# Kernel tuning notes

Hardware: AMD Instinct MI355X
Metric: run time of the kernel (lower is better)

## Reference

```python
import jax, jax.numpy as jnp
import numpy as np

B, S, H = 1, 4096, 3584
NQ, NKV, D = 16, 8, 256
N_REP = NQ // NKV  # GQA repeat factor = 2
WINDOW = 2048
SOFTCAP = 50.0
THETA = 10000.0
SCALE = D ** -0.5


def rotate_half(x):
    h = x.shape[-1] // 2
    return jnp.concatenate([-x[..., h:], x[..., :h]], axis=-1)


def setup_inputs() -> dict:
    key = jax.random.key(0)
    k0, k1, k2, k3, k4 = jax.random.split(key, 5)
    return {
        "hidden_states": jax.random.normal(k0, (B, S, H), jnp.float32),
        "wq": jax.random.normal(k1, (H, NQ * D), jnp.float32) / np.sqrt(H).astype(np.float32),
        "wk": jax.random.normal(k2, (H, NKV * D), jnp.float32) / np.sqrt(H).astype(np.float32),
        "wv": jax.random.normal(k3, (H, NKV * D), jnp.float32) / np.sqrt(H).astype(np.float32),
        "wo": jax.random.normal(k4, (NQ * D, H), jnp.float32) / np.sqrt(NQ * D).astype(np.float32),
        "position_ids": jnp.arange(S, dtype=jnp.int64 if jax.config.jax_enable_x64 else jnp.int32)[None, :],
    }


def reference(hidden_states, wq, wk, wv, wo, position_ids):
    b, s, h = hidden_states.shape
    # QKV projections (no bias, per attention_bias=False)
    q = (hidden_states @ wq).reshape(b, s, NQ, D).transpose(0, 2, 1, 3)   # [b, nq, s, d]
    k = (hidden_states @ wk).reshape(b, s, NKV, D).transpose(0, 2, 1, 3)  # [b, nkv, s, d]
    v = (hidden_states @ wv).reshape(b, s, NKV, D).transpose(0, 2, 1, 3)

    # Rotary embeddings (Gemma2RotaryEmbedding): freqs duplicated, rotate_half form
    pos = position_ids.astype(jnp.float32)                         # [b, s]
    inv_freq = 1.0 / (THETA ** (jnp.arange(0, D, 2, dtype=jnp.float32) / D))  # [d/2]
    freqs = pos[..., None] * inv_freq                              # [b, s, d/2]
    emb = jnp.concatenate([freqs, freqs], axis=-1)                 # [b, s, d]
    cos = jnp.cos(emb)[:, None, :, :]                              # [b, 1, s, d]
    sin = jnp.sin(emb)[:, None, :, :]
    q = q * cos + rotate_half(q) * sin
    k = k * cos + rotate_half(k) * sin

    # GQA: repeat_kv (repeat_interleave over head dim)
    k = jnp.repeat(k, N_REP, axis=1)  # [b, nq, s, d]
    v = jnp.repeat(v, N_REP, axis=1)

    # scaled scores + logit softcapping
    scores = jnp.einsum('bhqd,bhkd->bhqk', q, k) * SCALE
    scores = SOFTCAP * jnp.tanh(scores / SOFTCAP)

    # causal + sliding-window mask built from positions
    qpos = position_ids[:, None, :, None]  # [b,1,s,1]
    kpos = position_ids[:, None, None, :]  # [b,1,1,s]
    visible = (kpos <= qpos) & (kpos > qpos - WINDOW)
    scores = jnp.where(visible, scores, jnp.finfo(scores.dtype).min)

    attn = jax.nn.softmax(scores, axis=-1)
    out = jnp.einsum('bhqk,bhkd->bhqd', attn, v)      # [b, nq, s, d]
    out = out.transpose(0, 2, 1, 3).reshape(b, s, NQ * D)
    return out @ wo                                    # [b, s, h]
```

## Files before the change

kernel.cpp:

```cpp
#include <hip/hip_runtime.h>
#include <hip/hip_bf16.h>
#include <cstdint>
#include <cstddef>

#define DEVFN __device__ __forceinline__

typedef __attribute__((ext_vector_type(4))) float f32x4;
typedef __attribute__((ext_vector_type(8))) short bf16x8;
typedef __attribute__((ext_vector_type(4))) short short4v;

static constexpr int S = 4096;
static constexpr int H = 3584;
static constexpr int NQ = 16;
static constexpr int NKV = 8;
static constexpr int D = 256;
static constexpr int WINDOW = 2048;
static constexpr float SCALE = 0.0625f;

DEVFN unsigned short f2bf(float f) {
  union { float f; uint32_t u; } x; x.f = f;
  uint32_t u = x.u;
  u += 0x7fffu + ((u >> 16) & 1u);
  return (unsigned short)(u >> 16);
}
DEVFN float bf2f(unsigned short h) {
  union { uint32_t u; float f; } x; x.u = ((uint32_t)h) << 16;
  return x.f;
}

DEVFN void load_lds16(const void* g, void* l) {
  __builtin_amdgcn_global_load_lds((const __attribute__((address_space(1))) void*)g,
                                   (__attribute__((address_space(3))) void*)l,
                                   16, 0, 0);
}

__global__ __launch_bounds__(256) void cast_hs_kernel(const float* __restrict__ in,
                                                      unsigned short* __restrict__ out) {
  int i = (blockIdx.x * 256 + threadIdx.x) * 4;
  float4 v = *(const float4*)(in + i);
  short4v o;
  o[0] = (short)f2bf(v.x); o[1] = (short)f2bf(v.y);
  o[2] = (short)f2bf(v.z); o[3] = (short)f2bf(v.w);
  *(short4v*)(out + i) = o;
}

__global__ void transpose_cast_kernel(const float* __restrict__ in, unsigned short* __restrict__ out,
                                      int rows, int cols, int out_ld) {
  __shared__ float tile[32][33];
  int r0 = blockIdx.y * 32, c0 = blockIdx.x * 32;
  int tx = threadIdx.x, ty = threadIdx.y;
#pragma unroll
  for (int j = 0; j < 32; j += 8)
    tile[ty + j][tx] = in[(size_t)(r0 + ty + j) * cols + (c0 + tx)];
  __syncthreads();
#pragma unroll
  for (int j = 0; j < 32; j += 8)
    out[(size_t)(c0 + ty + j) * out_ld + (r0 + tx)] = f2bf(tile[tx][ty + j]);
}

__global__ __launch_bounds__(256) void rope_table_kernel(float* __restrict__ cs) {
  int idx = blockIdx.x * 256 + threadIdx.x;
  int s = idx >> 7, i = idx & 127;
  float inv = 1.0f / powf(10000.0f, (float)i * (1.0f / 128.0f));
  float f = (float)s * inv;
  cs[idx] = cosf(f);
  cs[(S * 128) + idx] = sinf(f);
}

__global__ __launch_bounds__(256) void rope_apply_kernel(unsigned short* __restrict__ q,
                                                         unsigned short* __restrict__ k,
                                                         const float* __restrict__ cs) {
  int idx = blockIdx.x * 256 + threadIdx.x;
  int i4 = (idx & 31) * 4;
  int s = (idx >> 5) & (S - 1);
  int hh = idx >> 17;
  unsigned short* base = (hh < NQ) ? (q + ((size_t)hh * S + s) * D)
                                   : (k + ((size_t)(hh - NQ) * S + s) * D);
  float4 c  = *(const float4*)(cs + (s << 7) + i4);
  float4 sn = *(const float4*)(cs + (S * 128) + (s << 7) + i4);
  short4v a = *(short4v*)(base + i4);
  short4v b = *(short4v*)(base + i4 + 128);
  short4v o1, o2;
  o1[0] = (short)f2bf(bf2f((unsigned short)a[0]) * c.x - bf2f((unsigned short)b[0]) * sn.x);
  o1[1] = (short)f2bf(bf2f((unsigned short)a[1]) * c.y - bf2f((unsigned short)b[1]) * sn.y);
  o1[2] = (short)f2bf(bf2f((unsigned short)a[2]) * c.z - bf2f((unsigned short)b[2]) * sn.z);
  o1[3] = (short)f2bf(bf2f((unsigned short)a[3]) * c.w - bf2f((unsigned short)b[3]) * sn.w);
  o2[0] = (short)f2bf(bf2f((unsigned short)b[0]) * c.x + bf2f((unsigned short)a[0]) * sn.x);
  o2[1] = (short)f2bf(bf2f((unsigned short)b[1]) * c.y + bf2f((unsigned short)a[1]) * sn.y);
  o2[2] = (short)f2bf(bf2f((unsigned short)b[2]) * c.z + bf2f((unsigned short)a[2]) * sn.z);
  o2[3] = (short)f2bf(bf2f((unsigned short)b[3]) * c.w + bf2f((unsigned short)a[3]) * sn.w);
  *(short4v*)(base + i4) = o1;
  *(short4v*)(base + i4 + 128) = o2;
}

DEVFN void gemm256_mainloop(const unsigned short* __restrict__ A,
                            const unsigned short* __restrict__ Bt,
                            int Kdim, int lda, int ldb, int row0, int col0,
                            char* lds, f32x4 acc[8][4]) {
  const int tid = threadIdx.x, lane = tid & 63;
  const int w = tid >> 6;
  const int wm = w >> 2, wn = w & 3;
  const int NT = Kdim >> 6;

  const int u = ((tid & 7) * 16) ^ (((tid >> 3) & 7) << 4);
  const int srow = (tid >> 3) + (u >> 6) * 128;
  const int sc = (u & 63) >> 1;

  const unsigned short* aSrc = A + (size_t)(row0 + srow) * lda + sc;
  const unsigned short* bSrc = Bt + (size_t)(col0 + srow) * ldb + sc;
  const size_t aj = (size_t)64 * lda, bj = (size_t)64 * ldb;

  char* const dA = lds + tid * 16;
  char* const dB = lds + 32768 + tid * 16;

  const int aoff = (lane & 15) * 128 + ((((lane >> 4) * 16) + wm * 64) ^ ((lane & 7) << 4));
  const int boff = ((wn & 1) * 64 + (lane & 15)) * 128 +
                   ((((lane >> 4) * 16) + (wn >> 1) * 64) ^ ((lane & 7) << 4));

#define STAGE_A(kt2, kh) do { \
    char* d_ = dA + (((kt2) & 1) << 16) + ((kh) << 14); \
    const unsigned short* s_ = aSrc + (kt2) * 64 + (kh) * 32; \
    load_lds16(s_, d_); load_lds16(s_ + aj, d_ + 8192); } while (0)
#define STAGE_B(kt2, kh) do { \
    char* d_ = dB + (((kt2) & 1) << 16) + ((kh) << 14); \
    const unsigned short* s_ = bSrc + (kt2) * 64 + (kh) * 32; \
    load_lds16(s_, d_); load_lds16(s_ + bj, d_ + 8192); } while (0)

  STAGE_A(0, 0); STAGE_B(0, 0); STAGE_A(0, 1); STAGE_B(0, 1);
  if (NT > 1) { STAGE_A(1, 0); STAGE_B(1, 0); }
  asm volatile("s_waitcnt vmcnt(4)" ::: "memory");
  __builtin_amdgcn_s_barrier();
  asm volatile("" ::: "memory");

  for (int kt = 0; kt < NT; ++kt) {
    const char* lA = lds + ((kt & 1) << 16) + aoff;
    const char* lB = lds + ((kt & 1) << 16) + 32768 + boff;
    bf16x8 bfr[4];
#pragma unroll
    for (int ph = 0; ph < 4; ++ph) {
      const int kh = ph >> 1;
      const int mh = ph & 1;
      bf16x8 af[4];
#pragma unroll
      for (int j = 0; j < 4; ++j)
        af[j] = *(const bf16x8*)(lA + (kh << 14) + (mh * 4 + j) * 2048);
      if (mh == 0) {
#pragma unroll
        for (int n = 0; n < 4; ++n)
          bfr[n] = *(const bf16x8*)(lB + (kh << 14) + n * 2048);
      }
      if (ph == 0)      { if (kt + 1 < NT) STAGE_A(kt + 1, 1); }
      else if (ph == 1) { if (kt + 1 < NT) STAGE_B(kt + 1, 1); }
      else if (ph == 2) { if (kt + 2 < NT) STAGE_A(kt + 2, 0); }
      else              { if (kt + 2 < NT) STAGE_B(kt + 2, 0); }

      asm volatile("" ::: "memory");
      __builtin_amdgcn_s_barrier();
      asm volatile("" ::: "memory");
      __builtin_amdgcn_s_setprio(1);
#pragma unroll
      for (int j = 0; j < 4; ++j)
#pragma unroll
        for (int n = 0; n < 4; ++n)
          acc[mh * 4 + j][n] =
              __builtin_amdgcn_mfma_f32_16x16x32_bf16(af[j], bfr[n], acc[mh * 4 + j][n], 0, 0, 0);
      __builtin_amdgcn_s_setprio(0);
      if (ph == 3) {
        if (kt < NT - 2) asm volatile("s_waitcnt vmcnt(4)" ::: "memory");
        else             asm volatile("s_waitcnt vmcnt(0)" ::: "memory");
      }
      asm volatile("" ::: "memory");
      __builtin_amdgcn_s_barrier();
      asm volatile("" ::: "memory");
    }
  }
#undef STAGE_A
#undef STAGE_B
}

__global__ __launch_bounds__(512, 2) void gemm_qkv_kernel(const unsigned short* __restrict__ A,
                                                          const unsigned short* __restrict__ Bt,
                                                          unsigned short* __restrict__ qb,
                                                          unsigned short* __restrict__ kbuf,
                                                          unsigned short* __restrict__ vtb) {
  extern __shared__ char lds[];
  int bid = blockIdx.x;
  bid = (bid & 7) * 64 + (bid >> 3);
  const int bx = bid & 15, by = bid >> 4;
  const int row0 = bx * 256, col0 = by * 256;
  f32x4 acc[8][4];
  f32x4 z = {0.f, 0.f, 0.f, 0.f};
#pragma unroll
  for (int m = 0; m < 8; ++m)
#pragma unroll
    for (int n = 0; n < 4; ++n) acc[m][n] = z;

  gemm256_mainloop(A, Bt, H, H, H, row0, col0, lds, acc);

  const int lane = threadIdx.x & 63, w = threadIdx.x >> 6;
  const int wm = w >> 2, wn = w & 3;
  const int rbase = row0 + wm * 128 + (lane >> 4) * 4;
  const int cbase = col0 + wn * 64 + (lane & 15);
  if (col0 < 4096) {
#pragma unroll
    for (int m = 0; m < 8; ++m)
#pragma unroll
      for (int n = 0; n < 4; ++n)
#pragma unroll
        for (int r = 0; r < 4; ++r) {
          int row = rbase + m * 16 + r;
          int col = cbase + n * 16;
          qb[((size_t)(col >> 8) * S + row) * D + (col & 255)] = f2bf(acc[m][n][r]);
        }
  } else if (col0 < 6144) {
#pragma unroll
    for (int m = 0; m < 8; ++m)
#pragma unroll
      for (int n = 0; n < 4; ++n)
#pragma unroll
        for (int r = 0; r < 4; ++r) {
          int row = rbase + m * 16 + r;
          int c2 = cbase + n * 16 - 4096;
          kbuf[((size_t)(c2 >> 8) * S + row) * D + (c2 & 255)] = f2bf(acc[m][n][r]);
        }
  } else {
#pragma unroll
    for (int m = 0; m < 8; ++m)
#pragma unroll
      for (int n = 0; n < 4; ++n)
#pragma unroll
        for (int r = 0; r < 4; ++r) {
          int row = rbase + m * 16 + r;
          int c3 = cbase + n * 16 - 6144;
          vtb[((size_t)(c3 >> 8) * D + (c3 & 255)) * S + row] = f2bf(acc[m][n][r]);
        }
  }
}

__global__ __launch_bounds__(512, 2) void gemm_out_kernel(const unsigned short* __restrict__ A,
                                                          const unsigned short* __restrict__ Bt,
                                                          float* __restrict__ C) {
  extern __shared__ char lds[];
  int bid = blockIdx.x;
  bid = (bid & 7) * 28 + (bid >> 3);
  const int bx = bid & 15, by = bid >> 4;
  const int row0 = bx * 256, col0 = by * 256;
  f32x4 acc[8][4];
  f32x4 z = {0.f, 0.f, 0.f, 0.f};
#pragma unroll
  for (int m = 0; m < 8; ++m)
#pragma unroll
    for (int n = 0; n < 4; ++n) acc[m][n] = z;

  gemm256_mainloop(A, Bt, NQ * D, NQ * D, NQ * D, row0, col0, lds, acc);

  const int lane = threadIdx.x & 63, w = threadIdx.x >> 6;
  const int wm = w >> 2, wn = w & 3;
  const int rbase = row0 + wm * 128 + (lane >> 4) * 4;
  const int cbase = col0 + wn * 64 + (lane & 15);
#pragma unroll
  for (int m = 0; m < 8; ++m)
#pragma unroll
    for (int n = 0; n < 4; ++n)
#pragma unroll
      for (int r = 0; r < 4; ++r)
        C[(size_t)(rbase + m * 16 + r) * H + cbase + n * 16] = acc[m][n][r];
}

__global__ __launch_bounds__(256) void attn_kernel(const unsigned short* __restrict__ q,
                                                   const unsigned short* __restrict__ kk_,
                                                   const unsigned short* __restrict__ vt,
                                                   unsigned short* __restrict__ aout) {
  __shared__ __align__(16) char kl[2][16384];
  __shared__ __align__(16) char vl[2][16384];
  __shared__ __align__(16) char pl[4096];
  const int tid = threadIdx.x, lane = tid & 63, w = tid >> 6;
  const int h = blockIdx.y, hv = h >> 1;
  const int q0 = blockIdx.x * 64;
  const int ql = lane & 15;
  const int grp = lane >> 4;
  const int qg = q0 + w * 16 + ql;

  bf16x8 qf[8];
  const unsigned short* qrow = q + ((size_t)h * S + qg) * D;
#pragma unroll
  for (int t = 0; t < 8; ++t)
    qf[t] = *(const bf16x8*)(qrow + t * 32 + grp * 8);

  f32x4 oacc[16];
  f32x4 z = {0.f, 0.f, 0.f, 0.f};
#pragma unroll
  for (int i = 0; i < 16; ++i) oacc[i] = z;
  float lrun = 0.0f;

  int lo = q0 - (WINDOW - 1); if (lo < 0) lo = 0;
  const int kb0 = lo & ~31;
  const int kend = q0 + 32;

  const unsigned short* kbase = kk_ + (size_t)hv * S * D;
  const unsigned short* vbase = vt + (size_t)hv * D * S;
  int koff[4], voff[4];
#pragma unroll
  for (int j = 0; j < 4; ++j) {
    int c = w + 4 * j;
    int key = c * 2 + (lane >> 5);
    int colK = (((lane & 31) * 16) ^ ((key & 7) << 4)) >> 1;
    koff[j] = key * D + colK;
    int dd = c * 16 + (lane >> 2);
    int colV = (((lane & 3) * 16) ^ (((dd >> 1) & 3) << 4)) >> 1;
    voff[j] = dd * S + colV;
  }

  auto stage = [&](int buf, int kb) {
#pragma unroll
    for (int j = 0; j < 4; ++j) {
      int c = w + 4 * j;
      load_lds16(kbase + (size_t)kb * D + koff[j], &kl[buf][c * 1024]);
      load_lds16(vbase + kb + voff[j], &vl[buf][c * 1024]);
    }
  };

  stage(0, kb0);
  int cur = 0;
  const int psw = ((ql >> 1) & 3) << 4;
  char* pw = pl + w * 1024;

  for (int kb = kb0; kb <= kend; kb += 32) {
    __syncthreads();
    if (kb + 32 <= kend) stage(cur ^ 1, kb + 32);

    f32x4 sacc[2];
    sacc[0] = z; sacc[1] = z;
#pragma unroll
    for (int mt = 0; mt < 2; ++mt) {
      const int krow = mt * 16 + ql;
      const char* kbp = kl[cur] + krow * 512;
      const int sw = (krow & 7) << 4;
#pragma unroll
      for (int t = 0; t < 8; ++t) {
        bf16x8 a = *(const bf16x8*)(kbp + ((t * 64 + grp * 16) ^ sw));
        sacc[mt] = __builtin_amdgcn_mfma_f32_16x16x32_bf16(a, qf[t], sacc[mt], 0, 0, 0);
      }
    }

    float pv[8];
#pragma unroll
    for (int i = 0; i < 8; ++i) {
      float x = sacc[i >> 2][i & 3];
      float e = __expf(x * (SCALE / 25.0f));
      float rc = __builtin_amdgcn_rcpf(e + 1.0f);
      pv[i] = __expf(rc * -100.0f);
    }
    if (kb + 31 > q0) {
#pragma unroll
      for (int i = 0; i < 8; ++i) {
        int key = kb + (i >> 2) * 16 + grp * 4 + (i & 3);
        if (key > qg) pv[i] = 0.0f;
      }
    } else if (kb < q0 - (WINDOW - 64)) {
#pragma unroll
      for (int i = 0; i < 8; ++i) {
        int key = kb + (i >> 2) * 16 + grp * 4 + (i & 3);
        if (key <= qg - WINDOW) pv[i] = 0.0f;
      }
    }
#pragma unroll
    for (int i = 0; i < 8; ++i) lrun += pv[i];

#pragma unroll
    for (int mt = 0; mt < 2; ++mt) {
      short4v pk;
      pk[0] = (short)f2bf(pv[mt * 4 + 0]);
      pk[1] = (short)f2bf(pv[mt * 4 + 1]);
      pk[2] = (short)f2bf(pv[mt * 4 + 2]);
      pk[3] = (short)f2bf(pv[mt * 4 + 3]);
      *(short4v*)(pw + ql * 64 + ((mt * 32 + grp * 8) ^ psw)) = pk;
    }
    asm volatile("s_waitcnt lgkmcnt(0)" ::: "memory");
    bf16x8 pb = *(const bf16x8*)(pw + ql * 64 + ((grp * 16) ^ psw));

#pragma unroll
    for (int nt = 0; nt < 16; ++nt) {
      int dr = nt * 16 + ql;
      bf16x8 va = *(const bf16x8*)(vl[cur] + dr * 64 + ((grp * 16) ^ (((dr >> 1) & 3) << 4)));
      oacc[nt] = __builtin_amdgcn_mfma_f32_16x16x32_bf16(va, pb, oacc[nt], 0, 0, 0);
    }
    cur ^= 1;
  }

  lrun += __shfl_xor(lrun, 16);
  lrun += __shfl_xor(lrun, 32);
  lrun = fmaxf(lrun, 1e-35f);
  float rl = 1.0f / lrun;
  unsigned short* orow = aout + (size_t)qg * (NQ * D) + h * D;
#pragma unroll
  for (int nt = 0; nt < 16; ++nt) {
    short4v o;
    o[0] = (short)f2bf(oacc[nt][0] * rl);
    o[1] = (short)f2bf(oacc[nt][1] * rl);
    o[2] = (short)f2bf(oacc[nt][2] * rl);
    o[3] = (short)f2bf(oacc[nt][3] * rl);
    *(short4v*)(orow + nt * 16 + grp * 4) = o;
  }
}

extern "C" void kernel_launch(void* const* d_in, const int* in_sizes, int n_in,
                              void* d_out, int out_size, void* d_ws, size_t ws_size,
                              hipStream_t stream) {
  const float* hs = (const float*)d_in[0];
  const float* wq = (const float*)d_in[1];
  const float* wk = (const float*)d_in[2];
  const float* wv = (const float*)d_in[3];
  const float* wo = (const float*)d_in[4];
  float* out = (float*)d_out;

  char* ws = (char*)d_ws;
  size_t off = 0;
  auto alloc = [&](size_t bytes) {
    char* p = ws + off;
    off += (bytes + 255) & ~(size_t)255;
    return p;
  };
  unsigned short* hsb   = (unsigned short*)alloc((size_t)S * H * 2);
  unsigned short* wqkvT = (unsigned short*)alloc((size_t)8192 * H * 2);
  unsigned short* woT   = (unsigned short*)alloc((size_t)H * 4096 * 2);
  unsigned short* qb    = (unsigned short*)alloc((size_t)NQ * S * D * 2);
  unsigned short* kbuf  = (unsigned short*)alloc((size_t)NKV * S * D * 2);
  unsigned short* vtb   = (unsigned short*)alloc((size_t)NKV * D * S * 2);
  unsigned short* aob   = (unsigned short*)alloc((size_t)S * NQ * D * 2);
  float*          cs    = (float*)alloc((size_t)S * 128 * 2 * 4);
  if (off > ws_size) return;

  dim3 tb(32, 8);
  cast_hs_kernel<<<(S * H) / 1024, 256, 0, stream>>>(hs, hsb);
  transpose_cast_kernel<<<dim3(4096 / 32, H / 32), tb, 0, stream>>>(wq, wqkvT, H, 4096, H);
  transpose_cast_kernel<<<dim3(2048 / 32, H / 32), tb, 0, stream>>>(wk, wqkvT + (size_t)4096 * H, H, 2048, H);
  transpose_cast_kernel<<<dim3(2048 / 32, H / 32), tb, 0, stream>>>(wv, wqkvT + (size_t)6144 * H, H, 2048, H);
  transpose_cast_kernel<<<dim3(H / 32, 4096 / 32), tb, 0, stream>>>(wo, woT, 4096, H, 4096);
  rope_table_kernel<<<(S * 128) / 256, 256, 0, stream>>>(cs);
  gemm_qkv_kernel<<<512, 512, 131072, stream>>>(hsb, wqkvT, qb, kbuf, vtb);
  rope_apply_kernel<<<((NQ + NKV) * S * 32) / 256, 256, 0, stream>>>(qb, kbuf, cs);
  attn_kernel<<<dim3(S / 64, NQ), 256, 0, stream>>>(qb, kbuf, vtb, aob);
  gemm_out_kernel<<<224, 512, 131072, stream>>>(aob, woT, out);
}
```

Measured before the change: 650.3 us.

## Double query rows per attention block to reuse K/V tiles across two query subtiles

Each attention block now covers 128 queries instead of 64, and each wave processes two 16-row query subtiles. Every K and V fragment read from LDS feeds MFMAs for both subtiles, which halves K/V global traffic and LDS reads per query. The costs are higher register pressure from two output accumulator sets (launch_bounds now requests 2 blocks per SIMD), half as many blocks in the grid, and more wasted work on fully masked tiles because the key range per block is wider.

```diff
diff --git a/kernel.cpp b/kernel.cpp
--- a/kernel.cpp
+++ b/kernel.cpp
@@ -267,35 +267,40 @@
         C[(size_t)(rbase + m * 16 + r) * H + cbase + n * 16] = acc[m][n][r];
 }
 
-__global__ __launch_bounds__(256) void attn_kernel(const unsigned short* __restrict__ q,
-                                                   const unsigned short* __restrict__ kk_,
-                                                   const unsigned short* __restrict__ vt,
-                                                   unsigned short* __restrict__ aout) {
+__global__ __launch_bounds__(256, 2) void attn_kernel(const unsigned short* __restrict__ q,
+                                                      const unsigned short* __restrict__ kk_,
+                                                      const unsigned short* __restrict__ vt,
+                                                      unsigned short* __restrict__ aout) {
   __shared__ __align__(16) char kl[2][16384];
   __shared__ __align__(16) char vl[2][16384];
-  __shared__ __align__(16) char pl[4096];
+  __shared__ __align__(16) char pl[8192];
   const int tid = threadIdx.x, lane = tid & 63, w = tid >> 6;
   const int h = blockIdx.y, hv = h >> 1;
-  const int q0 = blockIdx.x * 64;
+  const int q0 = blockIdx.x * 128;
   const int ql = lane & 15;
   const int grp = lane >> 4;
-  const int qg = q0 + w * 16 + ql;
-
-  bf16x8 qf[8];
-  const unsigned short* qrow = q + ((size_t)h * S + qg) * D;
-#pragma unroll
-  for (int t = 0; t < 8; ++t)
-    qf[t] = *(const bf16x8*)(qrow + t * 32 + grp * 8);
-
-  f32x4 oacc[16];
+  const int qw = q0 + w * 32;
+
+  bf16x8 qf[2][8];
+#pragma unroll
+  for (int qs = 0; qs < 2; ++qs) {
+    const unsigned short* qrow = q + ((size_t)h * S + qw + qs * 16 + ql) * D;
+#pragma unroll
+    for (int t = 0; t < 8; ++t)
+      qf[qs][t] = *(const bf16x8*)(qrow + t * 32 + grp * 8);
+  }
+
+  f32x4 oacc[2][16];
   f32x4 z = {0.f, 0.f, 0.f, 0.f};
 #pragma unroll
-  for (int i = 0; i < 16; ++i) oacc[i] = z;
-  float lrun = 0.0f;
+  for (int qs = 0; qs < 2; ++qs)
+#pragma unroll
+    for (int i = 0; i < 16; ++i) oacc[qs][i] = z;
+  float lrun[2] = {0.0f, 0.0f};
 
   int lo = q0 - (WINDOW - 1); if (lo < 0) lo = 0;
   const int kb0 = lo & ~31;
-  const int kend = q0 + 32;
+  const int kend = q0 + 96;
 
   const unsigned short* kbase = kk_ + (size_t)hv * S * D;
   const unsigned short* vbase = vt + (size_t)hv * D * S;
@@ -323,84 +328,99 @@
   stage(0, kb0);
   int cur = 0;
   const int psw = ((ql >> 1) & 3) << 4;
-  char* pw = pl + w * 1024;
+  char* pw = pl + w * 2048;
+  const int ksw = (ql & 7) << 4;
 
   for (int kb = kb0; kb <= kend; kb += 32) {
     __syncthreads();
     if (kb + 32 <= kend) stage(cur ^ 1, kb + 32);
 
-    f32x4 sacc[2];
-    sacc[0] = z; sacc[1] = z;
-#pragma unroll
-    for (int mt = 0; mt < 2; ++mt) {
-      const int krow = mt * 16 + ql;
-      const char* kbp = kl[cur] + krow * 512;
-      const int sw = (krow & 7) << 4;
-#pragma unroll
-      for (int t = 0; t < 8; ++t) {
-        bf16x8 a = *(const bf16x8*)(kbp + ((t * 64 + grp * 16) ^ sw));
-        sacc[mt] = __builtin_amdgcn_mfma_f32_16x16x32_bf16(a, qf[t], sacc[mt], 0, 0, 0);
+    f32x4 sacc[2][2];
+    sacc[0][0] = z; sacc[0][1] = z; sacc[1][0] = z; sacc[1][1] = z;
+#pragma unroll
+    for (int t = 0; t < 8; ++t) {
+      bf16x8 af[2];
+#pragma unroll
+      for (int ms = 0; ms < 2; ++ms)
+        af[ms] = *(const bf16x8*)(kl[cur] + (ms * 16 + ql) * 512 + ((t * 64 + grp * 16) ^ ksw));
+#pragma unroll
+      for (int qs = 0; qs < 2; ++qs)
+#pragma unroll
+        for (int ms = 0; ms < 2; ++ms)
+          sacc[qs][ms] = __builtin_amdgcn_mfma_f32_16x16x32_bf16(af[ms], qf[qs][t], sacc[qs][ms], 0, 0, 0);
+    }
+
+#pragma unroll
+    for (int qs = 0; qs < 2; ++qs) {
+      const int qsb = qw + qs * 16;
+      const int qg = qsb + ql;
+      float pv[8];
+#pragma unroll
+      for (int i = 0; i < 8; ++i) {
+        float x = sacc[qs][i >> 2][i & 3];
+        float e = __expf(x * (SCALE / 25.0f));
+        float rc = __builtin_amdgcn_rcpf(e + 1.0f);
+        pv[i] = __expf(rc * -100.0f);
       }
-    }
-
-    float pv[8];
-#pragma unroll
-    for (int i = 0; i < 8; ++i) {
-      float x = sacc[i >> 2][i & 3];
-      float e = __expf(x * (SCALE / 25.0f));
-      float rc = __builtin_amdgcn_rcpf(e + 1.0f);
-      pv[i] = __expf(rc * -100.0f);
-    }
-    if (kb + 31 > q0) {
-#pragma unroll
-      for (int i = 0; i < 8; ++i) {
-        int key = kb + (i >> 2) * 16 + grp * 4 + (i & 3);
-        if (key > qg) pv[i] = 0.0f;
+      if (kb + 31 > qsb) {
+#pragma unroll
+        for (int i = 0; i < 8; ++i) {
+          int key = kb + (i >> 2) * 16 + grp * 4 + (i & 3);
+          if (key > qg) pv[i] = 0.0f;
+        }
+      } else if (kb < qsb - 2032) {
+#pragma unroll
+        for (int i = 0; i < 8; ++i) {
+          int key = kb + (i >> 2) * 16 + grp * 4 + (i & 3);
+          if (key <= qg - WINDOW) pv[i] = 0.0f;
+        }
       }
-    } else if (kb < q0 - (WINDOW - 64)) {
-#pragma unroll
-      for (int i = 0; i < 8; ++i) {
-        int key = kb + (i >> 2) * 16 + grp * 4 + (i & 3);
-        if (key <= qg - WINDOW) pv[i] = 0.0f;
+#pragma unroll
+      for (int i = 0; i < 8; ++i) lrun[qs] += pv[i];
+
+#pragma unroll
+      for (int ms = 0; ms < 2; ++ms) {
+        short4v pk;
+        pk[0] = (short)f2bf(pv[ms * 4 + 0]);
+        pk[1] = (short)f2bf(pv[ms * 4 + 1]);
+        pk[2] = (short)f2bf(pv[ms * 4 + 2]);
+        pk[3] = (short)f2bf(pv[ms * 4 + 3]);
+        *(short4v*)(pw + (qs * 16 + ql) * 64 + ((ms * 32 + grp * 8) ^ psw)) = pk;
       }
     }
-#pragma unroll
-    for (int i = 0; i < 8; ++i) lrun += pv[i];
-
-#pragma unroll
-    for (int mt = 0; mt < 2; ++mt) {
-      short4v pk;
-      pk[0] = (short)f2bf(pv[mt * 4 + 0]);
-      pk[1] = (short)f2bf(pv[mt * 4 + 1]);
-      pk[2] = (short)f2bf(pv[mt * 4 + 2]);
-      pk[3] = (short)f2bf(pv[mt * 4 + 3]);
-      *(short4v*)(pw + ql * 64 + ((mt * 32 + grp * 8) ^ psw)) = pk;
-    }
     asm volatile("s_waitcnt lgkmcnt(0)" ::: "memory");
-    bf16x8 pb = *(const bf16x8*)(pw + ql * 64 + ((grp * 16) ^ psw));
+    bf16x8 pb[2];
+#pragma unroll
+    for (int qs = 0; qs < 2; ++qs)
+      pb[qs] = *(const bf16x8*)(pw + (qs * 16 + ql) * 64 + ((grp * 16) ^ psw));
 
 #pragma unroll
     for (int nt = 0; nt < 16; ++nt) {
       int dr = nt * 16 + ql;
       bf16x8 va = *(const bf16x8*)(vl[cur] + dr * 64 + ((grp * 16) ^ (((dr >> 1) & 3) << 4)));
-      oacc[nt] = __builtin_amdgcn_mfma_f32_16x16x32_bf16(va, pb, oacc[nt], 0, 0, 0);
+      oacc[0][nt] = __builtin_amdgcn_mfma_f32_16x16x32_bf16(va, pb[0], oacc[0][nt], 0, 0, 0);
+      oacc[1][nt] = __builtin_amdgcn_mfma_f32_16x16x32_bf16(va, pb[1], oacc[1][nt], 0, 0, 0);
     }
     cur ^= 1;
   }
 
-  lrun += __shfl_xor(lrun, 16);
-  lrun += __shfl_xor(lrun, 32);
-  lrun = fmaxf(lrun, 1e-35f);
-  float rl = 1.0f / lrun;
-  unsigned short* orow = aout + (size_t)qg * (NQ * D) + h * D;
-#pragma unroll
-  for (int nt = 0; nt < 16; ++nt) {
-    short4v o;
-    o[0] = (short)f2bf(oacc[nt][0] * rl);
-    o[1] = (short)f2bf(oacc[nt][1] * rl);
-    o[2] = (short)f2bf(oacc[nt][2] * rl);
-    o[3] = (short)f2bf(oacc[nt][3] * rl);
-    *(short4v*)(orow + nt * 16 + grp * 4) = o;
+#pragma unroll
+  for (int qs = 0; qs < 2; ++qs) {
+    float l = lrun[qs];
+    l += __shfl_xor(l, 16);
+    l += __shfl_xor(l, 32);
+    l = fmaxf(l, 1e-35f);
+    float rl = 1.0f / l;
+    unsigned short* orow = aout + (size_t)(qw + qs * 16 + ql) * (NQ * D) + h * D;
+#pragma unroll
+    for (int nt = 0; nt < 16; ++nt) {
+      short4v o;
+      o[0] = (short)f2bf(oacc[qs][nt][0] * rl);
+      o[1] = (short)f2bf(oacc[qs][nt][1] * rl);
+      o[2] = (short)f2bf(oacc[qs][nt][2] * rl);
+      o[3] = (short)f2bf(oacc[qs][nt][3] * rl);
+      *(short4v*)(orow + nt * 16 + grp * 4) = o;
+    }
   }
 }
 
@@ -440,6 +460,6 @@
   rope_table_kernel<<<(S * 128) / 256, 256, 0, stream>>>(cs);
   gemm_qkv_kernel<<<512, 512, 131072, stream>>>(hsb, wqkvT, qb, kbuf, vtb);
   rope_apply_kernel<<<((NQ + NKV) * S * 32) / 256, 256, 0, stream>>>(qb, kbuf, cs);
-  attn_kernel<<<dim3(S / 64, NQ), 256, 0, stream>>>(qb, kbuf, vtb, aob);
+  attn_kernel<<<dim3(S / 128, NQ), 256, 0, stream>>>(qb, kbuf, vtb, aob);
   gemm_out_kernel<<<224, 512, 131072, stream>>>(aob, woT, out);
 }
```

Measured after the change: 621.9 us. -4.4%, faster.
